# Performance work log

Measured on AMD Instinct MI355X. Metric: run time of the kernel, lower is better.

The kernel has to match this reference:

```python
import jax, jax.numpy as jnp
import numpy as np

EPS = 1e-08
PARTIAL_NORM = 1.5
TOPK = 8
SELF_MOD_STEPS = 2


def _layernorm(x, g, b, eps=1e-05):
    mu = jnp.mean(x, axis=-1, keepdims=True)
    var = jnp.mean((x - mu) ** 2, axis=-1, keepdims=True)
    return (x - mu) / jnp.sqrt(var + eps) * g + b


def _spectral_normalize(w, iters=10):
    # mimic torch spectral_norm: divide by top singular value (power iteration)
    u = jnp.ones((w.shape[0],), w.dtype) / np.sqrt(w.shape[0])
    def step(u, _):
        v = w.T @ u
        v = v / (jnp.linalg.norm(v) + 1e-12)
        u2 = w @ v
        u2 = u2 / (jnp.linalg.norm(u2) + 1e-12)
        return u2, None
    u, _ = jax.lax.scan(step, u, None, length=iters)
    v = w.T @ u
    v = v / (jnp.linalg.norm(v) + 1e-12)
    sigma = u @ (w @ v)
    return w / sigma


def setup_inputs() -> dict:
    B, D, H, S, C = 8192, 2048, 1024, 3, 1000
    P = 1024  # proj_dim = ((max(H, D//2)+7)//8)*8
    key = jax.random.key(0)
    ks = jax.random.split(key, 16)
    x = jax.random.normal(ks[0], (B, D), jnp.float32)
    proj_w = jax.random.normal(ks[1], (P, D), jnp.float32) / np.sqrt(D)
    proj_b = jnp.zeros((P,), jnp.float32)
    ln_p_g = jnp.ones((P,), jnp.float32)
    ln_p_b = jnp.zeros((P,), jnp.float32)
    wf_w = jax.random.normal(ks[2], (S, 2 * H, P), jnp.float32) / np.sqrt(P)
    wf_w = jax.vmap(_spectral_normalize)(wf_w)
    wf_b = jax.random.normal(ks[3], (S, 2 * H), jnp.float32) * 0.02
    ln_g = jnp.ones((S, 2 * H), jnp.float32)
    ln_b = jnp.zeros((S, 2 * H), jnp.float32)
    temperature = jnp.ones((1,), jnp.float32)
    phases = jax.random.normal(ks[4], (S, 1), jnp.float32) * 0.5
    gate_w = jax.random.normal(ks[5], (H, H), jnp.float32) / np.sqrt(H)
    gate_b = jnp.zeros((H,), jnp.float32)
    cls_w1 = jax.random.normal(ks[6], (H, H), jnp.float32) / np.sqrt(H)
    cls_b1 = jnp.zeros((H,), jnp.float32)
    cls_w2 = jax.random.normal(ks[7], (C, H), jnp.float32) / np.sqrt(H)
    cls_b2 = jnp.zeros((C,), jnp.float32).at[1].set(0.75)
    return {"x": x, "proj_w": proj_w, "proj_b": proj_b, "ln_p_g": ln_p_g,
            "ln_p_b": ln_p_b, "wf_w": wf_w, "wf_b": wf_b, "ln_g": ln_g,
            "ln_b": ln_b, "temperature": temperature, "phases": phases,
            "gate_w": gate_w, "gate_b": gate_b, "cls_w1": cls_w1,
            "cls_b1": cls_b1, "cls_w2": cls_w2, "cls_b2": cls_b2}


def reference(x, proj_w, proj_b, ln_p_g, ln_p_b, wf_w, wf_b, ln_g, ln_b,
              temperature, phases, gate_w, gate_b, cls_w1, cls_b1, cls_w2, cls_b2):
    H = wf_w.shape[1] // 2
    # input projection (dropout is identity at eval)
    h = jax.nn.gelu(_layernorm(x @ proj_w.T + proj_b, ln_p_g, ln_p_b), approximate=False)
    # all wavefunctions at once: [B, S, 2H]
    out = jnp.einsum('bp,sep->bse', h, wf_w) + wf_b[None]
    out = _layernorm(out, ln_g[None], ln_b[None])
    out = jnp.exp(-out * out)  # ArcBell
    alpha, beta = out[..., :H], out[..., H:]
    norm_sq = jnp.sum(alpha ** 2 + beta ** 2, axis=-1, keepdims=True) + EPS
    factor = jnp.sqrt(PARTIAL_NORM ** 2 / norm_sq)
    alpha = alpha * factor
    beta = beta * factor
    phase = phases[None]  # [1, S, 1]
    c, s = jnp.cos(phase), jnp.sin(phase)
    wave_r = alpha * c - beta * s  # [B, S, H]
    wave_i = alpha * s + beta * c
    # cosine-similarity interference weights
    mean_real = jnp.mean(wave_r, axis=1)  # [B, H]
    mean_norm = jnp.sqrt(jnp.sum(mean_real ** 2, axis=-1, keepdims=True)) + EPS  # [B,1]
    wave_norms = jnp.sqrt(jnp.sum(wave_r ** 2, axis=-1, keepdims=True)) + EPS  # [B,S,1]
    dot = jnp.sum(wave_r * mean_real[:, None], axis=-1, keepdims=True)  # [B,S,1]
    cos_sim = (dot / (wave_norms * mean_norm[:, None]))[..., 0]  # [B,S]
    w = jax.nn.softmax(cos_sim / temperature, axis=1)[..., None]  # [B,S,1]
    sup_r = jnp.sum(wave_r * w, axis=1)  # [B,H]
    sup_i = jnp.sum(wave_i * w, axis=1)
    # self-modulation with leaky residual
    for _ in range(SELF_MOD_STEPS):
        mag = jnp.sqrt(sup_r ** 2 + sup_i ** 2 + EPS)
        gate = jax.nn.sigmoid(mag @ gate_w.T + gate_b)
        sup_r = sup_r * gate + sup_r * 0.1
        sup_i = sup_i * gate + sup_i * 0.1
    mag_sq = sup_r ** 2 + sup_i ** 2
    # top-k mask + scatter + renormalize
    _, inds = jax.lax.top_k(mag_sq, TOPK)
    rows = jnp.arange(mag_sq.shape[0])[:, None]
    mask = jnp.zeros_like(mag_sq).at[rows, inds].set(1.0)
    masked = mag_sq * mask
    probs = masked / (jnp.sum(masked, axis=-1, keepdims=True) + EPS)
    # classifier (dropout identity at eval)
    hid = jax.nn.gelu(probs @ cls_w1.T + cls_b1, approximate=False)
    logits = hid @ cls_w2.T + cls_b2
    return logits
```

## Files before the change

### kernel.cpp

```cpp
#include <hip/hip_runtime.h>
#include <cstdint>

typedef __attribute__((ext_vector_type(8))) __bf16 bf16x8;
typedef __attribute__((ext_vector_type(4))) __bf16 bf16x4;
typedef __attribute__((ext_vector_type(4))) float f32x4;
typedef unsigned long long u64;

__device__ __forceinline__ void gld_lds16(const void* g, void* l) {
  __builtin_amdgcn_global_load_lds(
      (const __attribute__((address_space(1))) void*)g,
      (__attribute__((address_space(3))) void*)l, 16, 0, 0);
}

__device__ __forceinline__ float block_sum(float v, float* scr) {
#pragma unroll
  for (int off = 32; off > 0; off >>= 1) v += __shfl_down(v, off, 64);
  const int w = threadIdx.x >> 6;
  __syncthreads();
  if ((threadIdx.x & 63) == 0) scr[w] = v;
  __syncthreads();
  float s = 0.f;
  const int nw = blockDim.x >> 6;
  for (int i = 0; i < nw; ++i) s += scr[i];
  return s;
}

template <int N>
__device__ __forceinline__ void block_sumN(float* v, float* scr) {
#pragma unroll
  for (int i = 0; i < N; ++i)
#pragma unroll
    for (int m = 1; m < 64; m <<= 1) v[i] += __shfl_xor(v[i], m, 64);
  const int w = threadIdx.x >> 6;
  __syncthreads();
  if ((threadIdx.x & 63) == 0)
#pragma unroll
    for (int i = 0; i < N; ++i) scr[w * N + i] = v[i];
  __syncthreads();
#pragma unroll
  for (int i = 0; i < N; ++i) {
    float s = 0.f;
    for (int ww = 0; ww < 4; ++ww) s += scr[ww * N + i];
    v[i] = s;
  }
}

__device__ __forceinline__ float gelu_fast(float x) {
  const float ax = fabsf(x) * 0.70710678118654752f;
  const float t = 1.f / (1.f + 0.3275911f * ax);
  const float e = __expf(-ax * ax);
  float poly = 1.061405429f;
  poly = poly * t - 1.453152027f;
  poly = poly * t + 1.421413741f;
  poly = poly * t - 0.284496736f;
  poly = poly * t + 0.254829592f;
  const float erfax = 1.f - poly * t * e;
  const float er = copysignf(erfax, x);
  return 0.5f * x * (1.f + er);
}

__global__ __launch_bounds__(256) void k_cast_bf16(const float* __restrict__ in,
                                                   __bf16* __restrict__ out) {
  const long i = ((long)blockIdx.x * 256 + threadIdx.x) * 4;
  f32x4 v = *(const f32x4*)(in + i);
  bf16x4 o = {(__bf16)v[0], (__bf16)v[1], (__bf16)v[2], (__bf16)v[3]};
  *(bf16x4*)(out + i) = o;
}

__global__ __launch_bounds__(256) void k_cast_weights(
    const float* __restrict__ pw, __bf16* __restrict__ w1b,
    const float* __restrict__ wfw, __bf16* __restrict__ wfwb,
    const float* __restrict__ gw, __bf16* __restrict__ gwb) {
  const int bid = blockIdx.x;
  const float* in;
  __bf16* out;
  long base;
  if (bid < 2048) { in = pw; out = w1b; base = (long)bid * 1024; }
  else if (bid < 8192) { in = wfw; out = wfwb; base = (long)(bid - 2048) * 1024; }
  else { in = gw; out = gwb; base = (long)(bid - 8192) * 1024; }
  const long i = base + threadIdx.x * 4;
  f32x4 v = *(const f32x4*)(in + i);
  bf16x4 o = {(__bf16)v[0], (__bf16)v[1], (__bf16)v[2], (__bf16)v[3]};
  *(bf16x4*)(out + i) = o;
}

__global__ __launch_bounds__(256) void k_cast_pad(const float* __restrict__ in,
                                                  __bf16* __restrict__ out,
                                                  int rows_real, int cols) {
  const long i = ((long)blockIdx.x * 256 + threadIdx.x) * 4;
  const int row = (int)(i / cols);
  const int col = (int)(i % cols);
  bf16x4 o;
  if (row < rows_real) {
    f32x4 v = *(const f32x4*)(in + (long)row * cols + col);
    o = (bf16x4){(__bf16)v[0], (__bf16)v[1], (__bf16)v[2], (__bf16)v[3]};
  } else {
    o = (bf16x4){(__bf16)0.f, (__bf16)0.f, (__bf16)0.f, (__bf16)0.f};
  }
  *(bf16x4*)(out + i) = o;
}

__global__ __launch_bounds__(256) void k_transpose1k(const float* __restrict__ in,
                                                     float* __restrict__ out) {
  __shared__ float t[32][33];
  const int tx = threadIdx.x & 31;
  const int ty = threadIdx.x >> 5;
  const int r0 = blockIdx.y * 32, c0 = blockIdx.x * 32;
#pragma unroll
  for (int k = 0; k < 4; ++k)
    t[ty + 8 * k][tx] = in[(long)(r0 + ty + 8 * k) * 1024 + c0 + tx];
  __syncthreads();
#pragma unroll
  for (int k = 0; k < 4; ++k)
    out[(long)(c0 + ty + 8 * k) * 1024 + r0 + tx] = t[tx][ty + 8 * k];
}

__global__ __launch_bounds__(512, 1) void k_gemm256_bt(
    const __bf16* __restrict__ A, const __bf16* __restrict__ B,
    const float* __restrict__ bias, __bf16* __restrict__ C,
    int M, int N, int K) {
  __shared__ __align__(16) __bf16 lds[2][2][256 * 64];
  const int tid = threadIdx.x;
  const int lane = tid & 63;
  const int wid = tid >> 6;
  const int wr = wid >> 2;
  const int wc = wid & 3;
  const int gx = gridDim.x, gy = gridDim.y;
  const int lin = blockIdx.y * gx + blockIdx.x;
  const int xcd = lin & 7;
  const int local = lin >> 3;
  const int byq = gy >> 3;
  const int bx = local / byq;
  const int by = xcd * byq + (local % byq);
  const int m0 = by * 256, n0 = bx * 256;
  const int fr = lane & 15;
  const int fx = lane >> 4;
  const int px = lane & 7;

  const __bf16* Abase = A + (long)m0 * K;
  const __bf16* Bbase = B + (long)n0 * K;

  auto stage_q = [&](int slot, int kt, int mat, int half) {
    const __bf16* src = (mat ? Bbase : Abase) + kt * 64;
#pragma unroll
    for (int q = 0; q < 2; ++q) {
      const int idx = q * 512 + tid;
      const int r = idx >> 3;
      const int pblk = idx & 7;
      const int row = half * 128 + r;
      const int lblk = pblk ^ (r & 7);
      gld_lds16(src + (long)row * K + lblk * 8,
                (char*)&lds[slot][mat][row * 64 + pblk * 8]);
    }
  };
  auto frag = [&](int slot, int mat, int row, int ks) -> bf16x8 {
    return *(const bf16x8*)&lds[slot][mat][row * 64 + ((((ks << 2) + fx) ^ px) << 3)];
  };

  f32x4 acc[8][4] = {};
  const int nt = K >> 6;
#pragma unroll
  for (int qp = 0; qp < 4; ++qp) stage_q(0, 0, qp >> 1, qp & 1);

  const int arow = wr * 128 + fr;
  const int brow = wc * 64 + fr;

  for (int t = 0; t < nt; ++t) {
    const int sc = t & 1, sn = sc ^ 1;
    if (t + 1 < nt) {
#pragma unroll
      for (int qp = 0; qp < 4; ++qp) stage_q(sn, t + 1, qp >> 1, qp & 1);
      asm volatile("s_waitcnt vmcnt(8)" ::: "memory");
    } else {
      asm volatile("s_waitcnt vmcnt(0)" ::: "memory");
    }
    __builtin_amdgcn_sched_barrier(0);
    __builtin_amdgcn_s_barrier();
    bf16x8 b0[4], b1[4];
#pragma unroll
    for (int j = 0; j < 4; ++j) {
      b0[j] = frag(sc, 1, brow + j * 16, 0);
      b1[j] = frag(sc, 1, brow + j * 16, 1);
    }
    __builtin_amdgcn_s_setprio(1);
#pragma unroll
    for (int im = 0; im < 8; ++im) {
      bf16x8 x0 = frag(sc, 0, arow + im * 16, 0);
      bf16x8 x1 = frag(sc, 0, arow + im * 16, 1);
#pragma unroll
      for (int j = 0; j < 4; ++j) {
        acc[im][j] = __builtin_amdgcn_mfma_f32_16x16x32_bf16(x0, b0[j], acc[im][j], 0, 0, 0);
        acc[im][j] = __builtin_amdgcn_mfma_f32_16x16x32_bf16(x1, b1[j], acc[im][j], 0, 0, 0);
      }
    }
    __builtin_amdgcn_s_setprio(0);
    __builtin_amdgcn_s_barrier();
  }

  __bf16* cb = (__bf16*)&lds[0][0][0];
  const int lm0 = wr * 128 + fx * 4;
  const int lc0 = wc * 64 + fr;
#pragma unroll
  for (int j = 0; j < 4; ++j) {
    const float bv = bias[n0 + lc0 + j * 16];
#pragma unroll
    for (int im = 0; im < 8; ++im)
#pragma unroll
      for (int r = 0; r < 4; ++r)
        cb[(lm0 + im * 16 + r) * 256 + lc0 + j * 16] = (__bf16)(acc[im][j][r] + bv);
  }
  __syncthreads();
#pragma unroll
  for (int q = 0; q < 16; ++q) {
    const int idx = q * 512 + tid;
    const int row = idx >> 5;
    const int c8 = (idx & 31) * 8;
    *(f32x4*)(C + (long)(m0 + row) * N + n0 + c8) = *(const f32x4*)(cb + row * 256 + c8);
  }
}

template <int EPI, int BM>
__global__ __launch_bounds__(256) void k_gemm_bt(
    const __bf16* __restrict__ A, const __bf16* __restrict__ B,
    const float* __restrict__ bias, void* __restrict__ Cout,
    int M, int N, int K, int Nreal,
    float* __restrict__ msq, __bf16* __restrict__ magOut) {
  constexpr int MR = BM / 32;
  constexpr int STAGE_B = (2 * BM * 32 + 2 * 128 * 32) * 2;
  constexpr int CB_B = BM * 64 * 4;
  constexpr int SMEM_B = STAGE_B > CB_B ? STAGE_B : CB_B;
  __shared__ __align__(16) char smem[SMEM_B];
  __bf16* As = (__bf16*)smem;
  __bf16* Bs = (__bf16*)(smem + (size_t)2 * BM * 32 * 2);
  float* cb = (float*)smem;
  const int tid = threadIdx.x;
  const int lane = tid & 63;
  const int wid = tid >> 6;
  const int wr = wid >> 1, wc = wid & 1;

  const int gx = gridDim.x, gy = gridDim.y;
  const int nwg = gx * gy;
  int bx, by;
  if ((nwg & 7) == 0) {
    const int lin = blockIdx.y * gx + blockIdx.x;
    const int cpx = nwg >> 3;
    const int w = (lin & 7) * cpx + (lin >> 3);
    bx = w / gy;
    by = w % gy;
  } else {
    bx = blockIdx.x;
    by = blockIdx.y;
  }
  const int m0 = by * BM;
  const int n0 = bx * 128;
  const int frow = lane & 15;
  const int fk = (lane >> 4) * 8;
  f32x4 acc[MR][4] = {};

  auto stage = [&](int buf, int k0) {
    const __bf16* Ab = A + (long)m0 * K + k0;
    const __bf16* Bb = B + (long)n0 * K + k0;
    __bf16* Asb = As + buf * BM * 32;
    __bf16* Bsb = Bs + buf * 128 * 32;
#pragma unroll
    for (int q = 0; q < BM / 64; ++q) {
      const int idx = q * 256 + tid;
      const int row = idx >> 2;
      const int col = (idx & 3) * 8;
      gld_lds16(Ab + (long)row * K + col, (char*)Asb + idx * 16);
    }
#pragma unroll
    for (int q = 0; q < 2; ++q) {
      const int idx = q * 256 + tid;
      const int row = idx >> 2;
      const int col = (idx & 3) * 8;
      gld_lds16(Bb + (long)row * K + col, (char*)Bsb + idx * 16);
    }
  };

  const int nt = K >> 5;
  int cur = 0;
  stage(0, 0);
  __syncthreads();
  for (int t = 0; t < nt; ++t) {
    if (t + 1 < nt) stage(cur ^ 1, (t + 1) << 5);
    bf16x8 af[MR], bfr[4];
#pragma unroll
    for (int i = 0; i < MR; ++i)
      af[i] = *(const bf16x8*)(As + cur * BM * 32 + (wr * (BM / 2) + i * 16 + frow) * 32 + fk);
#pragma unroll
    for (int i = 0; i < 4; ++i)
      bfr[i] = *(const bf16x8*)(Bs + cur * 128 * 32 + (wc * 64 + i * 16 + frow) * 32 + fk);
#pragma unroll
    for (int im = 0; im < MR; ++im)
#pragma unroll
      for (int in = 0; in < 4; ++in)
        acc[im][in] = __builtin_amdgcn_mfma_f32_16x16x32_bf16(af[im], bfr[in],
                                                              acc[im][in], 0, 0, 0);
    __syncthreads();
    cur ^= 1;
  }

  if (EPI == 0 || EPI == 6 || EPI == 7) {
#pragma unroll 1
    for (int h = 0; h < 2; ++h) {
      __syncthreads();
      if (wc == h) {
#pragma unroll
        for (int in = 0; in < 4; ++in) {
          const int col = n0 + h * 64 + in * 16 + frow;
          const float bv = (col < Nreal) ? bias[col] : 0.f;
          const int lcc = in * 16 + frow;
#pragma unroll
          for (int im = 0; im < MR; ++im)
#pragma unroll
            for (int r = 0; r < 4; ++r) {
              const float v = acc[im][in][r] + bv;
              float sv;
              if (EPI == 0) {
                sv = v;
              } else {
                const float f = 1.f / (1.f + __expf(-v)) + 0.1f;
                sv = f * f;
              }
              cb[(wr * (BM / 2) + (lane >> 4) * 4 + im * 16 + r) * 64 + lcc] = sv;
            }
        }
      }
      __syncthreads();
#pragma unroll
      for (int q = 0; q < BM / 16; ++q) {
        const int idx = q * 256 + tid;
        const int row = idx >> 4;
        const int c4 = (idx & 15) * 4;
        const int gc = n0 + h * 64 + c4;
        if (EPI == 0) {
          if (gc < Nreal)
            *(f32x4*)((float*)Cout + (long)(m0 + row) * Nreal + gc) =
                *(const f32x4*)(cb + row * 64 + c4);
        } else {
          const long gix = (long)(m0 + row) * Nreal + gc;
          f32x4 m = *(const f32x4*)(msq + gix);
          const f32x4 f2 = *(const f32x4*)(cb + row * 64 + c4);
          m[0] *= f2[0]; m[1] *= f2[1]; m[2] *= f2[2]; m[3] *= f2[3];
          *(f32x4*)(msq + gix) = m;
          if (EPI == 6) {
            bf16x4 mg = {(__bf16)sqrtf(m[0] + 1e-8f), (__bf16)sqrtf(m[1] + 1e-8f),
                         (__bf16)sqrtf(m[2] + 1e-8f), (__bf16)sqrtf(m[3] + 1e-8f)};
            *(bf16x4*)(magOut + gix) = mg;
          }
        }
      }
    }
  } else {
    const int crow0 = m0 + wr * (BM / 2) + (lane >> 4) * 4;
    const int ccol0 = n0 + wc * 64 + (lane & 15);
#pragma unroll
    for (int in = 0; in < 4; ++in) {
      const int col = ccol0 + in * 16;
      if (col >= Nreal) continue;
      const float bv = bias[col];
#pragma unroll
      for (int im = 0; im < MR; ++im) {
#pragma unroll
        for (int r = 0; r < 4; ++r) {
          const long row = crow0 + im * 16 + r;
          ((__bf16*)Cout)[row * Nreal + col] = (__bf16)(acc[im][in][r] + bv);
        }
      }
    }
  }
}

__global__ __launch_bounds__(256) void k_ln_gelu(const float* __restrict__ y,
                                                 const float* __restrict__ g,
                                                 const float* __restrict__ b,
                                                 __bf16* __restrict__ h) {
  __shared__ float scr[8];
  const int tid = threadIdx.x;
  const long row = blockIdx.x;
  const float* yr = y + row * 1024;
  f32x4 v = *(const f32x4*)(yr + tid * 4);
  float ls = v[0] + v[1] + v[2] + v[3];
  const float mu = block_sum(ls, scr) * (1.f / 1024.f);
  float lss = 0.f;
#pragma unroll
  for (int j = 0; j < 4; ++j) {
    const float d = v[j] - mu;
    lss += d * d;
  }
  const float var = block_sum(lss, scr) * (1.f / 1024.f);
  const float rstd = rsqrtf(var + 1e-5f);
  bf16x4 o;
#pragma unroll
  for (int j = 0; j < 4; ++j) {
    const int c = tid * 4 + j;
    const float t = (v[j] - mu) * rstd * g[c] + b[c];
    o[j] = (__bf16)gelu_fast(t);
  }
  *(bf16x4*)(h + row * 1024 + tid * 4) = o;
}

__global__ __launch_bounds__(256) void k_stage_c(
    const __bf16* __restrict__ outb, const float* __restrict__ ln_g,
    const float* __restrict__ ln_b, const float* __restrict__ phases,
    const float* __restrict__ temp, float* __restrict__ msq,
    __bf16* __restrict__ mag0, int b0) {
  __shared__ float scr[24];
  const int t = threadIdx.x;
  const long b = blockIdx.x;
  float wr[3][4], wi[3][4];

#pragma unroll 1
  for (int s = 0; s < 3; ++s) {
    const __bf16* src = outb + b * 6144 + s * 2048;
    const bf16x4 va = *(const bf16x4*)(src + t * 4);
    const bf16x4 vb = *(const bf16x4*)(src + 1024 + t * 4);
    float xa[4], xb[4];
    float red[2] = {0.f, 0.f};
#pragma unroll
    for (int j = 0; j < 4; ++j) {
      xa[j] = (float)va[j];
      xb[j] = (float)vb[j];
      red[0] += xa[j] + xb[j];
      red[1] += xa[j] * xa[j] + xb[j] * xb[j];
    }
    block_sumN<2>(red, scr);
    const float mu = red[0] * (1.f / 2048.f);
    const float var = red[1] * (1.f / 2048.f) - mu * mu;
    const float rstd = rsqrtf(var + 1e-5f);

    const f32x4 ga = *(const f32x4*)(ln_g + s * 2048 + t * 4);
    const f32x4 ba = *(const f32x4*)(ln_b + s * 2048 + t * 4);
    const f32x4 gb = *(const f32x4*)(ln_g + s * 2048 + 1024 + t * 4);
    const f32x4 bb = *(const f32x4*)(ln_b + s * 2048 + 1024 + t * 4);
    float ag[4], bg[4];
    float nsq[1] = {0.f};
#pragma unroll
    for (int j = 0; j < 4; ++j) {
      const float ya = (xa[j] - mu) * rstd * ga[j] + ba[j];
      const float yb = (xb[j] - mu) * rstd * gb[j] + bb[j];
      ag[j] = __expf(-ya * ya);
      bg[j] = __expf(-yb * yb);
      nsq[0] += ag[j] * ag[j] + bg[j] * bg[j];
    }
    block_sumN<1>(nsq, scr);
    const float factor = sqrtf(2.25f / (nsq[0] + 1e-8f));
    const float ph = phases[s];
    const float cs = __cosf(ph), sn = __sinf(ph);
#pragma unroll
    for (int j = 0; j < 4; ++j) {
      const float a = ag[j] * factor;
      const float b2 = bg[j] * factor;
      wr[s][j] = a * cs - b2 * sn;
      wi[s][j] = a * sn + b2 * cs;
    }
  }

  float mr[4];
  float pmn[1] = {0.f};
#pragma unroll
  for (int j = 0; j < 4; ++j) {
    const float m = (wr[0][j] + wr[1][j] + wr[2][j]) * (1.f / 3.f);
    mr[j] = m;
    pmn[0] += m * m;
  }
  block_sumN<1>(pmn, scr);
  const float mnorm = sqrtf(pmn[0]) + 1e-8f;

  float dw[6] = {0.f, 0.f, 0.f, 0.f, 0.f, 0.f};
#pragma unroll
  for (int j = 0; j < 4; ++j) {
    dw[0] += wr[0][j] * mr[j]; dw[1] += wr[0][j] * wr[0][j];
    dw[2] += wr[1][j] * mr[j]; dw[3] += wr[1][j] * wr[1][j];
    dw[4] += wr[2][j] * mr[j]; dw[5] += wr[2][j] * wr[2][j];
  }
  block_sumN<6>(dw, scr);
  const float T = temp[0];
  const float c0 = dw[0] / ((sqrtf(dw[1]) + 1e-8f) * mnorm) / T;
  const float c1 = dw[2] / ((sqrtf(dw[3]) + 1e-8f) * mnorm) / T;
  const float c2 = dw[4] / ((sqrtf(dw[5]) + 1e-8f) * mnorm) / T;
  const float mx = fmaxf(c0, fmaxf(c1, c2));
  const float e0 = __expf(c0 - mx), e1 = __expf(c1 - mx), e2 = __expf(c2 - mx);
  const float inv = 1.f / (e0 + e1 + e2);
  const float w0 = e0 * inv, w1 = e1 * inv, w2 = e2 * inv;

  const long base = (long)(b0 + b) * 1024 + t * 4;
  f32x4 m2o;
  bf16x4 mgo;
#pragma unroll
  for (int j = 0; j < 4; ++j) {
    const float sr = wr[0][j] * w0 + wr[1][j] * w1 + wr[2][j] * w2;
    const float si = wi[0][j] * w0 + wi[1][j] * w1 + wi[2][j] * w2;
    const float m2 = sr * sr + si * si;
    m2o[j] = m2;
    mgo[j] = (__bf16)sqrtf(m2 + 1e-8f);
  }
  *(f32x4*)(msq + base) = m2o;
  *(bf16x4*)(mag0 + base) = mgo;
}

__global__ __launch_bounds__(256) void k_topk_cls1(
    const float* __restrict__ msq,
    const float* __restrict__ w1t, const float* __restrict__ b1,
    __bf16* __restrict__ hid) {
  __shared__ u64 candk[32];
  __shared__ u64 selk_s[8];
  __shared__ float ssum_s;
  const int tid = threadIdx.x;
  const int lane = tid & 63;
  const int wv = tid >> 6;
  const long b = blockIdx.x;

  f32x4 mv = *(const f32x4*)(msq + b * 1024 + tid * 4);
  u64 key[4];
#pragma unroll
  for (int j = 0; j < 4; ++j)
    key[j] = ((u64)__float_as_uint(mv[j]) << 32) | (unsigned)(~(unsigned)(tid * 4 + j));
  u64 lm = key[0];
  int jm = 0;
#pragma unroll
  for (int j = 1; j < 4; ++j)
    if (key[j] > lm) { lm = key[j]; jm = j; }

#pragma unroll 1
  for (int it = 0; it < 8; ++it) {
    u64 bk = lm;
#pragma unroll
    for (int m = 1; m < 64; m <<= 1) {
      const u64 ok = __shfl_xor(bk, m, 64);
      bk = ok > bk ? ok : bk;
    }
    if (lane == 0) candk[wv * 8 + it] = bk;
    if (bk == lm) {
      key[jm] = 0ULL;
      lm = key[0]; jm = 0;
#pragma unroll
      for (int j = 1; j < 4; ++j)
        if (key[j] > lm) { lm = key[j]; jm = j; }
    }
  }
  __syncthreads();

  if (wv == 0) {
    u64 ck = (lane < 32) ? candk[lane] : 0ULL;
    float ss = 0.f;
#pragma unroll 1
    for (int it = 0; it < 8; ++it) {
      u64 bk = ck;
#pragma unroll
      for (int m = 1; m < 64; m <<= 1) {
        const u64 ok = __shfl_xor(bk, m, 64);
        bk = ok > bk ? ok : bk;
      }
      if (ck == bk) ck = 0ULL;
      if (lane == 0) {
        selk_s[it] = bk;
        ss += __uint_as_float((unsigned)(bk >> 32));
      }
    }
    if (lane == 0) ssum_s = ss;
  }
  __syncthreads();

  const float denom = 1.f / (ssum_s + 1e-8f);
  float p[8];
  int idx[8];
#pragma unroll
  for (int k = 0; k < 8; ++k) {
    const u64 kk = selk_s[k];
    p[k] = __uint_as_float((unsigned)(kk >> 32)) * denom;
    idx[k] = (int)(~(unsigned)kk & 1023u);
  }

  const int o0 = tid * 4;
  float acc0 = b1[o0], acc1 = b1[o0 + 1], acc2 = b1[o0 + 2], acc3 = b1[o0 + 3];
#pragma unroll
  for (int k = 0; k < 8; ++k) {
    const f32x4 wrow = *(const f32x4*)(w1t + (long)idx[k] * 1024 + o0);
    acc0 += p[k] * wrow[0];
    acc1 += p[k] * wrow[1];
    acc2 += p[k] * wrow[2];
    acc3 += p[k] * wrow[3];
  }
  bf16x4 o = {(__bf16)gelu_fast(acc0), (__bf16)gelu_fast(acc1),
              (__bf16)gelu_fast(acc2), (__bf16)gelu_fast(acc3)};
  *(bf16x4*)(hid + b * 1024 + o0) = o;
}

extern "C" void kernel_launch(void* const* d_in, const int* in_sizes, int n_in,
                              void* d_out, int out_size, void* d_ws, size_t ws_size,
                              hipStream_t stream) {
  const float* x      = (const float*)d_in[0];
  const float* proj_w = (const float*)d_in[1];
  const float* proj_b = (const float*)d_in[2];
  const float* ln_p_g = (const float*)d_in[3];
  const float* ln_p_b = (const float*)d_in[4];
  const float* wf_w   = (const float*)d_in[5];
  const float* wf_b   = (const float*)d_in[6];
  const float* ln_g   = (const float*)d_in[7];
  const float* ln_b   = (const float*)d_in[8];
  const float* temperature = (const float*)d_in[9];
  const float* phases = (const float*)d_in[10];
  const float* gate_w = (const float*)d_in[11];
  const float* gate_b = (const float*)d_in[12];
  const float* cls_w1 = (const float*)d_in[13];
  const float* cls_b1 = (const float*)d_in[14];
  const float* cls_w2 = (const float*)d_in[15];
  const float* cls_b2 = (const float*)d_in[16];
  float* out = (float*)d_out;
  (void)in_sizes; (void)n_in; (void)out_size;

  char* ws = (char*)d_ws;
  const size_t MB = 1024 * 1024;

  if (ws_size >= 196 * MB) {
    __bf16* xb   = (__bf16*)(ws + 0);
    float*  msq  = (float*)(ws + 0);
    float*  y1   = (float*)(ws + 32 * MB);
    __bf16* mag0 = (__bf16*)(ws + 32 * MB);
    __bf16* mag1 = (__bf16*)(ws + 48 * MB);
    __bf16* outb = (__bf16*)(ws + 64 * MB);
    __bf16* hid  = (__bf16*)(ws + 64 * MB);
    float*  w1t  = (float*)(ws + 96 * MB);
    __bf16* hb   = (__bf16*)(ws + 160 * MB);
    __bf16* wfwb = (__bf16*)(ws + 176 * MB);
    __bf16* gwb  = (__bf16*)(ws + 188 * MB);
    __bf16* c2b  = (__bf16*)(ws + 190 * MB);
    __bf16* w1b  = (__bf16*)(ws + 192 * MB);

    k_cast_bf16<<<16384, 256, 0, stream>>>(x, xb);
    k_cast_weights<<<9216, 256, 0, stream>>>(proj_w, w1b, wf_w, wfwb, gate_w, gwb);
    k_cast_pad<<<1024, 256, 0, stream>>>(cls_w2, c2b, 1000, 1024);

    k_gemm_bt<0, 64><<<dim3(8, 128), 256, 0, stream>>>(xb, w1b, proj_b, y1, 8192, 1024, 2048, 1024, nullptr, nullptr);
    k_ln_gelu<<<8192, 256, 0, stream>>>(y1, ln_p_g, ln_p_b, hb);

    k_gemm256_bt<<<dim3(24, 32), 512, 0, stream>>>(hb, wfwb, wf_b, outb, 8192, 6144, 1024);
    k_stage_c<<<8192, 256, 0, stream>>>(outb, ln_g, ln_b, phases, temperature, msq, mag0, 0);

    k_transpose1k<<<dim3(32, 32), 256, 0, stream>>>(cls_w1, w1t);
    k_gemm_bt<6, 64><<<dim3(8, 128), 256, 0, stream>>>(mag0, gwb, gate_b, nullptr, 8192, 1024, 1024, 1024, msq, mag1);
    k_gemm_bt<7, 64><<<dim3(8, 128), 256, 0, stream>>>(mag1, gwb, gate_b, nullptr, 8192, 1024, 1024, 1024, msq, nullptr);

    k_topk_cls1<<<8192, 256, 0, stream>>>(msq, w1t, cls_b1, hid);
    k_gemm_bt<0, 64><<<dim3(8, 128), 256, 0, stream>>>(hid, c2b, cls_b2, out, 8192, 1024, 1024, 1000, nullptr, nullptr);
  } else {
    __bf16* xb   = (__bf16*)(ws + 0);
    float*  msq  = (float*)(ws + 0);
    float*  y1   = (float*)(ws + 32 * MB);
    __bf16* outc = (__bf16*)(ws + 32 * MB);
    __bf16* mag1 = (__bf16*)(ws + 32 * MB);
    __bf16* hid  = (__bf16*)(ws + 48 * MB);
    __bf16* w1b  = (__bf16*)(ws + 64 * MB);
    __bf16* mag0 = (__bf16*)(ws + 64 * MB);
    __bf16* wfwb = (__bf16*)(ws + 96 * MB);
    __bf16* hb   = (__bf16*)(ws + 108 * MB);
    float*  w1t  = (float*)(ws + 108 * MB);
    __bf16* gwb  = (__bf16*)(ws + 124 * MB);
    __bf16* c2b  = (__bf16*)(ws + 126 * MB);

    k_cast_bf16<<<16384, 256, 0, stream>>>(x, xb);
    k_cast_weights<<<9216, 256, 0, stream>>>(proj_w, w1b, wf_w, wfwb, gate_w, gwb);
    k_cast_pad<<<1024, 256, 0, stream>>>(cls_w2, c2b, 1000, 1024);

    k_gemm_bt<0, 64><<<dim3(8, 128), 256, 0, stream>>>(xb, w1b, proj_b, y1, 8192, 1024, 2048, 1024, nullptr, nullptr);
    k_ln_gelu<<<8192, 256, 0, stream>>>(y1, ln_p_g, ln_p_b, hb);

    for (int c = 0; c < 4; ++c) {
      k_gemm_bt<1, 128><<<dim3(48, 16), 256, 0, stream>>>(hb + (size_t)c * 2048 * 1024, wfwb, wf_b,
                                                          outc, 2048, 6144, 1024, 6144, nullptr, nullptr);
      k_stage_c<<<2048, 256, 0, stream>>>(outc, ln_g, ln_b, phases, temperature,
                                          msq, mag0, c * 2048);
    }

    k_transpose1k<<<dim3(32, 32), 256, 0, stream>>>(cls_w1, w1t);
    k_gemm_bt<6, 64><<<dim3(8, 128), 256, 0, stream>>>(mag0, gwb, gate_b, nullptr, 8192, 1024, 1024, 1024, msq, mag1);
    k_gemm_bt<7, 64><<<dim3(8, 128), 256, 0, stream>>>(mag1, gwb, gate_b, nullptr, 8192, 1024, 1024, 1024, msq, nullptr);

    k_topk_cls1<<<8192, 256, 0, stream>>>(msq, w1t, cls_b1, hid);
    k_gemm_bt<0, 64><<<dim3(8, 128), 256, 0, stream>>>(hid, c2b, cls_b2, out, 8192, 1024, 1024, 1000, nullptr, nullptr);
  }
}
```

Before: 452.8 us.

## Halve K-tile in 256x256 GEMM to cut LDS and raise occupancy

The 256x256 bf16 GEMM now stages K-slices of 32 instead of 64, halving the double-buffered LDS footprint (128KB to 64KB) and raising the launch-bounds hint to allow more blocks per CU. The swizzle and fragment indexing are adapted to the 32-wide rows. The epilogue now writes the output tile in two 128-row halves so it fits the smaller LDS buffer. The cost is twice as many loop iterations and barriers per K, fewer MFMAs per sync, and a launch-bounds hint of 4 that may force register pressure with the 128-float accumulator array.

```diff
diff --git a/kernel.cpp b/kernel.cpp
--- a/kernel.cpp
+++ b/kernel.cpp
@@ -115,11 +115,11 @@
     out[(long)(c0 + ty + 8 * k) * 1024 + r0 + tx] = t[tx][ty + 8 * k];
 }
 
-__global__ __launch_bounds__(512, 1) void k_gemm256_bt(
+__global__ __launch_bounds__(512, 4) void k_gemm256_bt(
     const __bf16* __restrict__ A, const __bf16* __restrict__ B,
     const float* __restrict__ bias, __bf16* __restrict__ C,
     int M, int N, int K) {
-  __shared__ __align__(16) __bf16 lds[2][2][256 * 64];
+  __shared__ __align__(16) __bf16 lds[2][2][256 * 32];
   const int tid = threadIdx.x;
   const int lane = tid & 63;
   const int wid = tid >> 6;
@@ -135,32 +135,33 @@
   const int m0 = by * 256, n0 = bx * 256;
   const int fr = lane & 15;
   const int fx = lane >> 4;
-  const int px = lane & 7;
+  const int px = (lane >> 1) & 3;
 
   const __bf16* Abase = A + (long)m0 * K;
   const __bf16* Bbase = B + (long)n0 * K;
 
-  auto stage_q = [&](int slot, int kt, int mat, int half) {
-    const __bf16* src = (mat ? Bbase : Abase) + kt * 64;
-#pragma unroll
-    for (int q = 0; q < 2; ++q) {
-      const int idx = q * 512 + tid;
-      const int r = idx >> 3;
-      const int pblk = idx & 7;
-      const int row = half * 128 + r;
-      const int lblk = pblk ^ (r & 7);
-      gld_lds16(src + (long)row * K + lblk * 8,
-                (char*)&lds[slot][mat][row * 64 + pblk * 8]);
+  auto stage_t = [&](int slot, int kt) {
+#pragma unroll
+    for (int mat = 0; mat < 2; ++mat) {
+      const __bf16* src = (mat ? Bbase : Abase) + kt * 32;
+#pragma unroll
+      for (int q = 0; q < 2; ++q) {
+        const int idx = q * 512 + tid;
+        const int r = idx >> 2;
+        const int pblk = idx & 3;
+        const int lblk = pblk ^ ((r >> 1) & 3);
+        gld_lds16(src + (long)r * K + lblk * 8,
+                  (char*)&lds[slot][mat][r * 32 + pblk * 8]);
+      }
     }
   };
-  auto frag = [&](int slot, int mat, int row, int ks) -> bf16x8 {
-    return *(const bf16x8*)&lds[slot][mat][row * 64 + ((((ks << 2) + fx) ^ px) << 3)];
+  auto frag = [&](int slot, int mat, int row) -> bf16x8 {
+    return *(const bf16x8*)&lds[slot][mat][row * 32 + ((fx ^ px) << 3)];
   };
 
   f32x4 acc[8][4] = {};
-  const int nt = K >> 6;
-#pragma unroll
-  for (int qp = 0; qp < 4; ++qp) stage_q(0, 0, qp >> 1, qp & 1);
+  const int nt = K >> 5;
+  stage_t(0, 0);
 
   const int arow = wr * 128 + fr;
   const int brow = wc * 64 + fr;
@@ -168,54 +169,54 @@
   for (int t = 0; t < nt; ++t) {
     const int sc = t & 1, sn = sc ^ 1;
     if (t + 1 < nt) {
-#pragma unroll
-      for (int qp = 0; qp < 4; ++qp) stage_q(sn, t + 1, qp >> 1, qp & 1);
-      asm volatile("s_waitcnt vmcnt(8)" ::: "memory");
+      stage_t(sn, t + 1);
+      asm volatile("s_waitcnt vmcnt(4)" ::: "memory");
     } else {
       asm volatile("s_waitcnt vmcnt(0)" ::: "memory");
     }
     __builtin_amdgcn_sched_barrier(0);
     __builtin_amdgcn_s_barrier();
-    bf16x8 b0[4], b1[4];
-#pragma unroll
-    for (int j = 0; j < 4; ++j) {
-      b0[j] = frag(sc, 1, brow + j * 16, 0);
-      b1[j] = frag(sc, 1, brow + j * 16, 1);
-    }
+    bf16x8 bfr[4];
+#pragma unroll
+    for (int j = 0; j < 4; ++j) bfr[j] = frag(sc, 1, brow + j * 16);
     __builtin_amdgcn_s_setprio(1);
 #pragma unroll
     for (int im = 0; im < 8; ++im) {
-      bf16x8 x0 = frag(sc, 0, arow + im * 16, 0);
-      bf16x8 x1 = frag(sc, 0, arow + im * 16, 1);
-#pragma unroll
-      for (int j = 0; j < 4; ++j) {
-        acc[im][j] = __builtin_amdgcn_mfma_f32_16x16x32_bf16(x0, b0[j], acc[im][j], 0, 0, 0);
-        acc[im][j] = __builtin_amdgcn_mfma_f32_16x16x32_bf16(x1, b1[j], acc[im][j], 0, 0, 0);
-      }
+      bf16x8 x0 = frag(sc, 0, arow + im * 16);
+#pragma unroll
+      for (int j = 0; j < 4; ++j)
+        acc[im][j] = __builtin_amdgcn_mfma_f32_16x16x32_bf16(x0, bfr[j], acc[im][j], 0, 0, 0);
     }
     __builtin_amdgcn_s_setprio(0);
     __builtin_amdgcn_s_barrier();
   }
 
   __bf16* cb = (__bf16*)&lds[0][0][0];
-  const int lm0 = wr * 128 + fx * 4;
+  const int lm0 = fx * 4;
   const int lc0 = wc * 64 + fr;
-#pragma unroll
-  for (int j = 0; j < 4; ++j) {
-    const float bv = bias[n0 + lc0 + j * 16];
-#pragma unroll
-    for (int im = 0; im < 8; ++im)
-#pragma unroll
-      for (int r = 0; r < 4; ++r)
-        cb[(lm0 + im * 16 + r) * 256 + lc0 + j * 16] = (__bf16)(acc[im][j][r] + bv);
-  }
-  __syncthreads();
-#pragma unroll
-  for (int q = 0; q < 16; ++q) {
-    const int idx = q * 512 + tid;
-    const int row = idx >> 5;
-    const int c8 = (idx & 31) * 8;
-    *(f32x4*)(C + (long)(m0 + row) * N + n0 + c8) = *(const f32x4*)(cb + row * 256 + c8);
+#pragma unroll 1
+  for (int h = 0; h < 2; ++h) {
+    __syncthreads();
+    if (wr == h) {
+#pragma unroll
+      for (int j = 0; j < 4; ++j) {
+        const float bv = bias[n0 + lc0 + j * 16];
+#pragma unroll
+        for (int im = 0; im < 8; ++im)
+#pragma unroll
+          for (int r = 0; r < 4; ++r)
+            cb[(lm0 + im * 16 + r) * 256 + lc0 + j * 16] = (__bf16)(acc[im][j][r] + bv);
+      }
+    }
+    __syncthreads();
+#pragma unroll
+    for (int q = 0; q < 8; ++q) {
+      const int idx = q * 512 + tid;
+      const int row = idx >> 5;
+      const int c8 = (idx & 31) * 8;
+      *(f32x4*)(C + (long)(m0 + h * 128 + row) * N + n0 + c8) =
+          *(const f32x4*)(cb + row * 256 + c8);
+    }
   }
 }
 
```

Measured after the change: 1.053 ms. +132.4%, slower.
